# Kernel tuning notes

Measured on AMD Instinct MI355X. Metric: run time of the kernel, lower is better.

The kernel has to match this reference:

```python
import jax, jax.numpy as jnp
import numpy as np

B, N, C, H = 4, 2048, 1024, 16
D = C // H  # 64, head dim
EPS = 1e-5


def layernorm(x):
    # non-affine LayerNorm over last axis (Normalize)
    mu = jnp.mean(x, axis=-1, keepdims=True)
    var = jnp.var(x, axis=-1, keepdims=True)
    return (x - mu) * jax.lax.rsqrt(var + EPS)


def rope(t):
    # t: (B, H, N, D). Standard 1D rotary over head dim.
    half = D // 2
    inv_freq = 1.0 / (10000.0 ** (jnp.arange(half, dtype=jnp.float32) / half))
    ang = jnp.arange(N, dtype=jnp.float32)[:, None] * inv_freq[None, :]  # (N, half)
    cos, sin = jnp.cos(ang), jnp.sin(ang)  # (N, half)
    t1, t2 = t[..., :half], t[..., half:]
    return jnp.concatenate([t1 * cos - t2 * sin, t1 * sin + t2 * cos], axis=-1)


def setup_inputs() -> dict:
    key = jax.random.key(0)
    ks = jax.random.split(key, 5)
    x = jax.random.normal(ks[0], (B, N, C), dtype=jnp.float32)
    emb = jax.random.normal(ks[1], (B, N, C), dtype=jnp.float32)
    emb_w = jax.random.normal(ks[2], (C, 2 * C), dtype=jnp.float32) * (1.0 / np.sqrt(C))
    emb_b = jnp.zeros((2 * C,), dtype=jnp.float32)
    proj_w = jax.random.normal(ks[3], (C, 3 * C), dtype=jnp.float32) * (1.0 / np.sqrt(C))
    out_w = jax.random.normal(ks[4], (C, C), dtype=jnp.float32) * 0.02  # zero_module at init; nonzero for testing
    return {"x": x, "emb": emb, "emb_w": emb_w, "emb_b": emb_b,
            "proj_w": proj_w, "out_w": out_w}


def reference(x, emb, emb_w, emb_b, proj_w, out_w):
    # FiLM-conditioned norm
    ss = emb @ emb_w + emb_b                 # (B, N, 2C)
    scale, shift = jnp.split(ss, 2, axis=-1)
    h = layernorm(x) * (1.0 + scale) + shift  # (B, N, C)
    # QKV projection; 'b n (qkv h d) -> qkv b h n d'
    qkv = (h @ proj_w).reshape(B, N, 3, H, D).transpose(2, 0, 3, 1, 4)
    q, k, v = qkv[0], qkv[1], qkv[2]          # (B, H, N, D)
    # per-head QK norm + RoPE
    q, k = rope(layernorm(q)), rope(layernorm(k))
    # SDPA (non-causal, no dropout)
    scores = jnp.einsum('bhnd,bhmd->bhnm', q, k) / jnp.sqrt(jnp.float32(D))
    attn = jax.nn.softmax(scores, axis=-1)
    o = jnp.einsum('bhnm,bhmd->bhnd', attn, v)  # (B, H, N, D)
    o = o.transpose(0, 2, 1, 3).reshape(B, N, C)
    return o + o @ out_w
```

## Files before the change

kernel.cpp:

```cpp
#include <hip/hip_runtime.h>
#include <hip/hip_bf16.h>
#include <cstdint>
#include <cstddef>

#define Bb 4
#define Nn 2048
#define Cc_ 1024
#define Hh 16
#define Dd 64
#define Mm (Bb*Nn)

typedef unsigned short u16;
typedef unsigned int u32;
typedef __attribute__((ext_vector_type(8))) short short8;
typedef __attribute__((ext_vector_type(4))) short s16x4;
typedef __attribute__((ext_vector_type(4))) float f32x4;
typedef __attribute__((ext_vector_type(16))) float f32x16;
typedef __attribute__((ext_vector_type(2))) float f32x2;
typedef __attribute__((ext_vector_type(4))) unsigned short u16x4;

__device__ __forceinline__ float bf2f(u16 v){ u32 u = ((u32)v)<<16; return __builtin_bit_cast(float, u); }
__device__ __forceinline__ u16 f2bf(float f){ u32 u = __builtin_bit_cast(u32, f); return (u16)((u + 0x7FFFu + ((u>>16)&1u))>>16); }

using gp_t = const __attribute__((address_space(1))) u32*;
using lp_t = __attribute__((address_space(3))) u32*;
__device__ __forceinline__ void gld16(const void* g, void* l){
  __builtin_amdgcn_global_load_lds((gp_t)g, (lp_t)l, 16, 0, 0);
}

__device__ __forceinline__ u32 cvtpk(float lo, float hi){
  u32 r; asm("v_cvt_pk_bf16_f32 %0, %1, %2" : "=v"(r) : "v"(lo), "v"(hi)); return r;
}

__global__ __launch_bounds__(256) void kT_cvt(const float* __restrict__ in, u16* __restrict__ out,
                                              int R, int Ncols){
  __shared__ float tile[64][65];
  const int c0 = blockIdx.x*64, r0 = blockIdx.y*64;
  const int t = threadIdx.x;
  #pragma unroll
  for(int i=0;i<16;i++){ int e = i*256 + t; int r = e>>6, c = e&63;
    tile[r][c] = in[(size_t)(r0+r)*Ncols + c0 + c]; }
  __syncthreads();
  #pragma unroll
  for(int i=0;i<16;i++){ int e = i*256 + t; int cc = e>>6, r = e&63;
    out[(size_t)(c0+cc)*R + r0 + r] = f2bf(tile[r][cc]); }
}

__global__ __launch_bounds__(256) void k_cvt(const float* __restrict__ in, u16* __restrict__ o, int n){
  int i = (blockIdx.x*256 + threadIdx.x)*4;
  if(i >= n) return;
  f32x4 v = *(const f32x4*)(in + i);
  u16x4 r;
  #pragma unroll
  for(int j=0;j<4;j++) r[j] = f2bf(v[j]);
  *(u16x4*)(o + i) = r;
}

__global__ __launch_bounds__(256) void k_ropetab(float* __restrict__ tab){
  int idx = blockIdx.x*256 + threadIdx.x;
  int n = idx>>5, i = idx&31;
  float invf = powf(10000.f, -(float)i*(1.f/32.f));
  float ang = (float)n * invf;
  float s_, c_;
  sincosf(ang, &s_, &c_);
  f32x2 cs; cs[0] = c_; cs[1] = s_;
  ((f32x2*)tab)[idx] = cs;
}

__global__ __launch_bounds__(256) void k_ln_mod(const float* __restrict__ x, const float* __restrict__ ss,
                                                u16* __restrict__ h){
  const int r = blockIdx.x, t = threadIdx.x;
  const float* xr = x + (size_t)r*Cc_;
  f32x4 xv = *(const f32x4*)(xr + t*4);
  float s = xv[0]+xv[1]+xv[2]+xv[3];
  float s2 = xv[0]*xv[0]+xv[1]*xv[1]+xv[2]*xv[2]+xv[3]*xv[3];
  #pragma unroll
  for(int off=1; off<64; off<<=1){ s += __shfl_xor(s, off); s2 += __shfl_xor(s2, off); }
  __shared__ float red[8];
  int w = t>>6, l = t&63;
  if(l==0){ red[w] = s; red[4+w] = s2; }
  __syncthreads();
  s = red[0]+red[1]+red[2]+red[3];
  s2 = red[4]+red[5]+red[6]+red[7];
  float mu = s * (1.f/Cc_);
  float rstd = rsqrtf(s2*(1.f/Cc_) - mu*mu + 1e-5f);
  f32x4 sc = *(const f32x4*)(ss + (size_t)r*2*Cc_ + t*4);
  f32x4 sh = *(const f32x4*)(ss + (size_t)r*2*Cc_ + Cc_ + t*4);
  u16x4 o;
  #pragma unroll
  for(int j=0;j<4;j++){ float hv = (xv[j]-mu)*rstd*(1.f+sc[j]) + sh[j]; o[j] = f2bf(hv); }
  *(u16x4*)(h + (size_t)r*Cc_ + t*4) = o;
}

__global__ __launch_bounds__(256) void k_lnrope(u16* __restrict__ qp, u16* __restrict__ kp,
                                                const float* __restrict__ tab){
  const int w = threadIdx.x>>6, l = threadIdx.x&63;
  const int row = blockIdx.x*4 + w;
  u16* p = (blockIdx.y ? kp : qp) + (size_t)row*Dd;
  const int n = row & (Nn-1);
  float v = bf2f(p[l]);
  float s = v, s2 = v*v;
  #pragma unroll
  for(int off=1; off<64; off<<=1){ s += __shfl_xor(s, off); s2 += __shfl_xor(s2, off); }
  float mu = s*(1.f/64.f);
  float rstd = rsqrtf(s2*(1.f/64.f) - mu*mu + 1e-5f);
  float tv = (v - mu)*rstd;
  float pv = __shfl_xor(tv, 32);
  f32x2 cs = ((const f32x2*)tab)[n*32 + (l&31)];
  float o = (l < 32) ? (tv*cs[0] - pv*cs[1]) : (pv*cs[1] + tv*cs[0]);
  p[l] = f2bf(o);
}

__global__ __launch_bounds__(256) void k_vT(const u16* __restrict__ v, u16* __restrict__ vt){
  __shared__ u32 tile[64][65];
  const int bh = blockIdx.y, n0 = blockIdx.x*64;
  const int t = threadIdx.x;
  const u16* src = v + ((size_t)bh*Nn + n0)*Dd;
  #pragma unroll
  for(int i=0;i<16;i++){ int e = i*256+t; tile[e>>6][e&63] = src[e]; }
  __syncthreads();
  #pragma unroll
  for(int i=0;i<16;i++){ int e = i*256+t; int d = e>>6, n = e&63;
    vt[((size_t)bh*Dd + d)*Nn + n0 + n] = (u16)tile[n][d]; }
}

template<int MODE>
__global__ __launch_bounds__(256) void k_gemm(
    const u16* __restrict__ A, const u16* __restrict__ BT, int K, int Nc,
    const float* __restrict__ bias, float* __restrict__ outf,
    u16* __restrict__ qo, u16* __restrict__ ko, u16* __restrict__ vo,
    const float* __restrict__ addend)
{
  __shared__ u16 sA[128*64];
  __shared__ u16 sB[128*64];
  const int t = threadIdx.x, w = t>>6;
  const int lr = t&15, lg = (t&63)>>4;
  const int row0 = blockIdx.y*128, col0 = blockIdx.x*128;
  const int wm = w>>1, wn = w&1;
  f32x4 acc[4][4] = {};
  for(int k0=0; k0<K; k0+=64){
    #pragma unroll
    for(int c=0;c<4;c++){
      int e = (c*256+t)*8;
      int r = e>>6, ch = (e>>3)&7;
      int sw = ((ch ^ (r&7))<<3);
      const u16* ga = A + (size_t)(row0+r)*K + k0 + sw;
      gld16(ga, (char*)sA + (c*256 + w*64)*16);
      const u16* gb = BT + (size_t)(col0+r)*K + k0 + sw;
      gld16(gb, (char*)sB + (c*256 + w*64)*16);
    }
    asm volatile("s_waitcnt vmcnt(0)" ::: "memory");
    __syncthreads();
    #pragma unroll
    for(int kk=0;kk<2;kk++){
      short8 af[4], bfr[4];
      #pragma unroll
      for(int mi=0;mi<4;mi++){
        int r = wm*64 + mi*16 + lr;
        af[mi] = *(const short8*)(sA + r*64 + (((kk*4+lg) ^ (r&7))<<3));
      }
      #pragma unroll
      for(int ni=0;ni<4;ni++){
        int r = wn*64 + ni*16 + lr;
        bfr[ni] = *(const short8*)(sB + r*64 + (((kk*4+lg) ^ (r&7))<<3));
      }
      #pragma unroll
      for(int mi=0;mi<4;mi++)
        #pragma unroll
        for(int ni=0;ni<4;ni++)
          acc[mi][ni] = __builtin_amdgcn_mfma_f32_16x16x32_bf16(af[mi], bfr[ni], acc[mi][ni], 0,0,0);
    }
    __syncthreads();
  }
  #pragma unroll
  for(int mi=0;mi<4;mi++){
    #pragma unroll
    for(int ni=0;ni<4;ni++){
      #pragma unroll
      for(int j=0;j<4;j++){
        int grow = row0 + wm*64 + mi*16 + lg*4 + j;
        int gcol = col0 + wn*64 + ni*16 + lr;
        float val = acc[mi][ni][j];
        if(MODE==0){
          outf[(size_t)grow*Nc + gcol] = val + bias[gcol];
        } else if(MODE==1){
          int tt = gcol>>10, hh = (gcol>>6)&15, dd = gcol&63;
          int b = grow>>11, n = grow&(Nn-1);
          size_t idx = (((size_t)(b*Hh+hh))*Nn + n)*Dd + dd;
          u16 bv = f2bf(val);
          if(tt==0) qo[idx]=bv; else if(tt==1) ko[idx]=bv; else vo[idx]=bv;
        } else {
          size_t idx = (size_t)grow*Nc + gcol;
          outf[idx] = val + addend[idx];
        }
      }
    }
  }
}

__global__ __launch_bounds__(256,3) void k_attn(
    const u16* __restrict__ Q, const u16* __restrict__ Kb,
    const u16* __restrict__ VT, u16* __restrict__ obf, float* __restrict__ of)
{
  __shared__ u16 sK[2][4096];
  __shared__ u16 sV[2][4096];
  const int t = threadIdx.x, w = t>>6, l = t&63;
  const int srow = l&31, hi = l>>5;
  const int id = blockIdx.x;
  const int bh = ((id&7)<<3) | ((id>>3)&7);
  const int q0 = (id>>6)*128;
  const u16* qb = Q  + (size_t)bh*Nn*Dd;
  const u16* kg = Kb + (size_t)bh*Nn*Dd;
  const u16* vg = VT + (size_t)bh*Dd*Nn;

  short8 qf[4];
  #pragma unroll
  for(int c=0;c<4;c++)
    qf[c] = *(const short8*)(qb + (size_t)(q0 + w*32 + srow)*Dd + c*16 + hi*8);

  f32x16 o0 = {}, o1 = {};
  float mrun = -3e38f, lsum = 0.f;
  const float cl2 = 0.18033688011112042f;

  const int grow8 = l>>3;
  const int gc = (l&7) ^ grow8;

  #define STAGE(buf, kt) {                                                        \
    _Pragma("unroll")                                                             \
    for(int i=0;i<4;i++){                                                         \
      int ci = w*4 + i;                                                           \
      if(ci < 8){                                                                 \
        int row = ci*8 + grow8;                                                   \
        gld16(kg + (size_t)((kt)+row)*Dd + gc*8, (char*)&sK[buf][0] + ci*1024);   \
      } else {                                                                    \
        int row = (ci-8)*8 + grow8;                                               \
        gld16(vg + (size_t)row*Nn + (kt) + gc*8, (char*)&sV[buf][0] + (ci-8)*1024);\
      }                                                                           \
    }                                                                             \
  }

  STAGE(0, 0);
  asm volatile("s_waitcnt vmcnt(0)" ::: "memory");
  __syncthreads();

  const int NT = Nn/64;
  for(int tt=0; tt<NT; ++tt){
    int buf = tt&1;
    if(tt+1 < NT) STAGE(buf^1, (tt+1)*64);

    f32x16 s0 = {}, s1 = {};
    const u16* skb = &sK[buf][0];
    #pragma unroll
    for(int c=0;c<4;c++){
      int ch = (c*2+hi) ^ (l&7);
      short8 kf0 = *(const short8*)(skb + srow*64 + ch*8);
      short8 kf1 = *(const short8*)(skb + (32+srow)*64 + ch*8);
      s0 = __builtin_amdgcn_mfma_f32_32x32x16_bf16(kf0, qf[c], s0, 0,0,0);
      s1 = __builtin_amdgcn_mfma_f32_32x32x16_bf16(kf1, qf[c], s1, 0,0,0);
    }

    float pm = -3e38f;
    #pragma unroll
    for(int r=0;r<16;r++) pm = fmaxf(pm, fmaxf(s0[r], s1[r]));
    pm = fmaxf(pm, __shfl_xor(pm, 32));
    pm *= cl2;
    if(!__all(pm <= mrun + 8.f)){
      float mn = fmaxf(mrun, pm);
      float al = exp2f(mrun - mn);
      mrun = mn; lsum *= al;
      #pragma unroll
      for(int r=0;r<16;r++){ o0[r] *= al; o1[r] *= al; }
    }
    float rs = 0.f;
    #pragma unroll
    for(int r=0;r<16;r++){
      float p0 = exp2f(__builtin_fmaf(s0[r], cl2, -mrun)); s0[r] = p0;
      float p1 = exp2f(__builtin_fmaf(s1[r], cl2, -mrun)); s1[r] = p1;
      rs += p0 + p1;
    }
    rs += __shfl_xor(rs, 32);
    lsum += rs;

    const u16* svb = &sV[buf][0];
    #pragma unroll
    for(int kb=0;kb<2;kb++){
      const f32x16& sp = kb ? s1 : s0;
      union { u32 wd[4]; short8 v; } pA, pB;
      pA.wd[0]=cvtpk(sp[0],sp[1]);   pA.wd[1]=cvtpk(sp[2],sp[3]);
      pA.wd[2]=cvtpk(sp[4],sp[5]);   pA.wd[3]=cvtpk(sp[6],sp[7]);
      pB.wd[0]=cvtpk(sp[8],sp[9]);   pB.wd[1]=cvtpk(sp[10],sp[11]);
      pB.wd[2]=cvtpk(sp[12],sp[13]); pB.wd[3]=cvtpk(sp[14],sp[15]);
      #pragma unroll
      for(int db=0;db<2;db++){
        const int vrow = db*32 + srow;
        const u16* vr = svb + vrow*64;
        const int x = l&7;
        union { s16x4 h[2]; short8 v; } vA, vB;
        vA.h[0] = *(const s16x4*)(vr + (((kb*4+0)^x)<<3) + hi*4);
        vA.h[1] = *(const s16x4*)(vr + (((kb*4+1)^x)<<3) + hi*4);
        vB.h[0] = *(const s16x4*)(vr + (((kb*4+2)^x)<<3) + hi*4);
        vB.h[1] = *(const s16x4*)(vr + (((kb*4+3)^x)<<3) + hi*4);
        if(db==0){
          o0 = __builtin_amdgcn_mfma_f32_32x32x16_bf16(vA.v, pA.v, o0, 0,0,0);
          o0 = __builtin_amdgcn_mfma_f32_32x32x16_bf16(vB.v, pB.v, o0, 0,0,0);
        } else {
          o1 = __builtin_amdgcn_mfma_f32_32x32x16_bf16(vA.v, pA.v, o1, 0,0,0);
          o1 = __builtin_amdgcn_mfma_f32_32x32x16_bf16(vB.v, pB.v, o1, 0,0,0);
        }
      }
    }
    asm volatile("s_waitcnt vmcnt(0)" ::: "memory");
    __syncthreads();
  }

  float rl = 1.0f / lsum;
  const int n = q0 + w*32 + srow;
  const int b = bh>>4, hh = bh&15;
  size_t base = ((size_t)(b*Nn + n))*Cc_ + hh*Dd;
  #pragma unroll
  for(int db=0;db<2;db++){
    const f32x16& oo = db ? o1 : o0;
    #pragma unroll
    for(int mb=0;mb<4;mb++){
      int d0 = db*32 + mb*8 + hi*4;
      f32x4 v4; u16x4 h4;
      #pragma unroll
      for(int j=0;j<4;j++){ float v = oo[mb*4+j]*rl; v4[j] = v; h4[j] = f2bf(v); }
      *(f32x4*)(of + base + d0) = v4;
      *(u16x4*)(obf + base + d0) = h4;
    }
  }
}

extern "C" void kernel_launch(void* const* d_in, const int* in_sizes, int n_in,
                              void* d_out, int out_size, void* d_ws, size_t ws_size,
                              hipStream_t stream){
  const float* x      = (const float*)d_in[0];
  const float* emb    = (const float*)d_in[1];
  const float* emb_w  = (const float*)d_in[2];
  const float* emb_b  = (const float*)d_in[3];
  const float* proj_w = (const float*)d_in[4];
  const float* out_w  = (const float*)d_in[5];
  float* out = (float*)d_out;
  char* ws = (char*)d_ws;
  size_t off = 0;
  auto alloc = [&](size_t bytes)->char*{ char* p = ws + off; off += (bytes+255)&~(size_t)255; return p; };

  u16*  embbf = (u16*)alloc((size_t)Mm*Cc_*2);
  u16*  wT_e  = (u16*)alloc((size_t)2*Cc_*Cc_*2);
  u16*  wT_p  = (u16*)alloc((size_t)3*Cc_*Cc_*2);
  u16*  wT_o  = (u16*)alloc((size_t)Cc_*Cc_*2);
  float* ss   = (float*)alloc((size_t)Mm*2*Cc_*4);
  u16*  h     = (u16*)alloc((size_t)Mm*Cc_*2);
  u16*  qB    = (u16*)alloc((size_t)Mm*Cc_*2);
  u16*  kB    = (u16*)alloc((size_t)Mm*Cc_*2);
  u16*  vB    = (u16*)alloc((size_t)Mm*Cc_*2);
  float* tab  = (float*)alloc((size_t)Nn*32*8);

  u16*  vT  = embbf;
  float* of  = ss;
  u16*  obf = (u16*)((char*)ss + (size_t)Mm*Cc_*4);

  kT_cvt<<<dim3(32,16),256,0,stream>>>(emb_w,  wT_e, Cc_, 2*Cc_);
  kT_cvt<<<dim3(48,16),256,0,stream>>>(proj_w, wT_p, Cc_, 3*Cc_);
  kT_cvt<<<dim3(16,16),256,0,stream>>>(out_w,  wT_o, Cc_, Cc_);
  k_cvt<<<8192,256,0,stream>>>(emb, embbf, Mm*Cc_);
  k_ropetab<<<256,256,0,stream>>>(tab);
  k_gemm<0><<<dim3(16,64),256,0,stream>>>(embbf, wT_e, Cc_, 2*Cc_, emb_b, ss,
                                          nullptr,nullptr,nullptr, nullptr);
  k_ln_mod<<<Mm,256,0,stream>>>(x, ss, h);
  k_gemm<1><<<dim3(24,64),256,0,stream>>>(h, wT_p, Cc_, 3*Cc_, nullptr, nullptr,
                                          qB, kB, vB, nullptr);
  k_lnrope<<<dim3(32768,2),256,0,stream>>>(qB, kB, tab);
  k_vT<<<dim3(32,64),256,0,stream>>>(vB, vT);
  k_attn<<<1024,256,0,stream>>>(qB, kB, vT, obf, of);
  k_gemm<2><<<dim3(8,64),256,0,stream>>>(obf, wT_o, Cc_, Cc_, nullptr, out,
                                         nullptr,nullptr,nullptr, of);
}
```

Measured before the change: 465.3 us.

## Unroll attention loop by two with precomputed LDS offsets; remap GEMM block order

The attention loop is unrolled by two so each buffer index is a compile-time constant. Per-lane swizzled LDS offsets for K and V are precomputed once, and each wave gets a single global pointer that advances by a fixed stride, which removes per-iteration address arithmetic and branching. The GEMM kernel also remaps its flat block id in groups of eight, likely to improve L2/XCD locality. The costs are more code and registers for the offset arrays, and the block remap assumes the block count divides by eight.

```diff
diff --git a/kernel.cpp b/kernel.cpp
--- a/kernel.cpp
+++ b/kernel.cpp
@@ -135,7 +135,11 @@
   __shared__ u16 sB[128*64];
   const int t = threadIdx.x, w = t>>6;
   const int lr = t&15, lg = (t&63)>>4;
-  const int row0 = blockIdx.y*128, col0 = blockIdx.x*128;
+  const int gx = gridDim.x;
+  const int nwg = gx*gridDim.y;
+  const int fid = blockIdx.y*gx + blockIdx.x;
+  const int sid = (fid&7)*(nwg>>3) + (fid>>3);
+  const int row0 = (sid/gx)*128, col0 = (sid%gx)*128;
   const int wm = w>>1, wn = w&1;
   f32x4 acc[4][4] = {};
   for(int k0=0; k0<K; k0+=64){
@@ -224,44 +228,43 @@
 
   const int grow8 = l>>3;
   const int gc = (l&7) ^ grow8;
-
-  #define STAGE(buf, kt) {                                                        \
-    _Pragma("unroll")                                                             \
-    for(int i=0;i<4;i++){                                                         \
-      int ci = w*4 + i;                                                           \
-      if(ci < 8){                                                                 \
-        int row = ci*8 + grow8;                                                   \
-        gld16(kg + (size_t)((kt)+row)*Dd + gc*8, (char*)&sK[buf][0] + ci*1024);   \
-      } else {                                                                    \
-        int row = (ci-8)*8 + grow8;                                               \
-        gld16(vg + (size_t)row*Nn + (kt) + gc*8, (char*)&sV[buf][0] + (ci-8)*1024);\
-      }                                                                           \
-    }                                                                             \
-  }
-
-  STAGE(0, 0);
-  asm volatile("s_waitcnt vmcnt(0)" ::: "memory");
-  __syncthreads();
-
-  const int NT = Nn/64;
-  for(int tt=0; tt<NT; ++tt){
-    int buf = tt&1;
-    if(tt+1 < NT) STAGE(buf^1, (tt+1)*64);
-
+  const int x7 = l&7;
+
+  int koff[4], voff[8];
+  #pragma unroll
+  for(int c=0;c<4;c++)  koff[c]  = srow*128 + (((c*2+hi)^x7)<<4);
+  #pragma unroll
+  for(int cc=0;cc<8;cc++) voff[cc] = srow*128 + ((cc^x7)<<4) + hi*8;
+
+  const u16* gst; int sI, adv;
+  if(w < 2){ gst = kg + (size_t)(w*4)*512 + grow8*64 + gc*8;        sI = 512;   adv = 4096; }
+  else     { gst = vg + ((size_t)(w*4-8)*8 + grow8)*Nn + gc*8;      sI = 16384; adv = 64;   }
+  char* myLds0 = (w < 2) ? ((char*)&sK[0][0] + w*4096) : ((char*)&sV[0][0] + (w-2)*4096);
+  char* myLds1 = myLds0 + 8192;
+
+  auto stage = [&](char* dst){
+    #pragma unroll
+    for(int i=0;i<4;i++)
+      gld16(gst + (size_t)i*sI, dst + i*1024);
+    gst += adv;
+  };
+
+  auto compute = [&](int BUF){
+    const char* sKb = (const char*)&sK[BUF][0];
+    const char* sVb = (const char*)&sV[BUF][0];
     f32x16 s0 = {}, s1 = {};
-    const u16* skb = &sK[buf][0];
     #pragma unroll
     for(int c=0;c<4;c++){
-      int ch = (c*2+hi) ^ (l&7);
-      short8 kf0 = *(const short8*)(skb + srow*64 + ch*8);
-      short8 kf1 = *(const short8*)(skb + (32+srow)*64 + ch*8);
+      short8 kf0 = *(const short8*)(sKb + koff[c]);
+      short8 kf1 = *(const short8*)(sKb + koff[c] + 4096);
       s0 = __builtin_amdgcn_mfma_f32_32x32x16_bf16(kf0, qf[c], s0, 0,0,0);
       s1 = __builtin_amdgcn_mfma_f32_32x32x16_bf16(kf1, qf[c], s1, 0,0,0);
     }
-
-    float pm = -3e38f;
-    #pragma unroll
-    for(int r=0;r<16;r++) pm = fmaxf(pm, fmaxf(s0[r], s1[r]));
+    float pm = fmaxf(s0[0], s0[1]);
+    #pragma unroll
+    for(int r=2;r<16;r+=2) pm = fmaxf(pm, fmaxf(s0[r], s0[r+1]));
+    #pragma unroll
+    for(int r=0;r<16;r+=2) pm = fmaxf(pm, fmaxf(s1[r], s1[r+1]));
     pm = fmaxf(pm, __shfl_xor(pm, 32));
     pm *= cl2;
     if(!__all(pm <= mrun + 8.f)){
@@ -280,8 +283,6 @@
     }
     rs += __shfl_xor(rs, 32);
     lsum += rs;
-
-    const u16* svb = &sV[buf][0];
     #pragma unroll
     for(int kb=0;kb<2;kb++){
       const f32x16& sp = kb ? s1 : s0;
@@ -292,14 +293,11 @@
       pB.wd[2]=cvtpk(sp[12],sp[13]); pB.wd[3]=cvtpk(sp[14],sp[15]);
       #pragma unroll
       for(int db=0;db<2;db++){
-        const int vrow = db*32 + srow;
-        const u16* vr = svb + vrow*64;
-        const int x = l&7;
         union { s16x4 h[2]; short8 v; } vA, vB;
-        vA.h[0] = *(const s16x4*)(vr + (((kb*4+0)^x)<<3) + hi*4);
-        vA.h[1] = *(const s16x4*)(vr + (((kb*4+1)^x)<<3) + hi*4);
-        vB.h[0] = *(const s16x4*)(vr + (((kb*4+2)^x)<<3) + hi*4);
-        vB.h[1] = *(const s16x4*)(vr + (((kb*4+3)^x)<<3) + hi*4);
+        vA.h[0] = *(const s16x4*)(sVb + voff[kb*4+0] + db*4096);
+        vA.h[1] = *(const s16x4*)(sVb + voff[kb*4+1] + db*4096);
+        vB.h[0] = *(const s16x4*)(sVb + voff[kb*4+2] + db*4096);
+        vB.h[1] = *(const s16x4*)(sVb + voff[kb*4+3] + db*4096);
         if(db==0){
           o0 = __builtin_amdgcn_mfma_f32_32x32x16_bf16(vA.v, pA.v, o0, 0,0,0);
           o0 = __builtin_amdgcn_mfma_f32_32x32x16_bf16(vB.v, pB.v, o0, 0,0,0);
@@ -309,6 +307,20 @@
         }
       }
     }
+  };
+
+  stage(myLds0);
+  asm volatile("s_waitcnt vmcnt(0)" ::: "memory");
+  __syncthreads();
+
+  #pragma unroll 1
+  for(int m=0;m<16;m++){
+    stage(myLds1);
+    compute(0);
+    asm volatile("s_waitcnt vmcnt(0)" ::: "memory");
+    __syncthreads();
+    if(m < 15) stage(myLds0);
+    compute(1);
     asm volatile("s_waitcnt vmcnt(0)" ::: "memory");
     __syncthreads();
   }
```

Measured after the change: 473.3 us. About the same (+1.7%).
